# Kernel optimization log

Hardware: AMD Instinct MI355X
Metric: run time of the kernel (lower is better)

The kernel has to match this reference:

```python
import jax, jax.numpy as jnp
import numpy as np

EMBED_DIM = 1024
NUM_HEADS = 16
HEAD_DIM = EMBED_DIM // NUM_HEADS
SCALING = HEAD_DIM ** -0.5
NEG_FILL = -1e30


def setup_inputs() -> dict:
    key = jax.random.key(0)
    k1, k2, k3 = jax.random.split(key, 3)
    T, B, E = 2048, 4, EMBED_DIM
    query = jax.random.normal(k1, (T, B, E), dtype=jnp.float32)
    key_padding_mask = jnp.zeros((B, T), dtype=bool)  # 1 = padded key
    # xavier_uniform-like init
    lim_in = (6.0 / (3 * E + E)) ** 0.5
    in_proj_weight = jax.random.uniform(k2, (3 * E, E), minval=-lim_in, maxval=lim_in, dtype=jnp.float32)
    in_proj_bias = jnp.zeros((3 * E,), dtype=jnp.float32)
    lim_out = (6.0 / (E + E)) ** 0.5
    out_w = jax.random.uniform(k3, (E, E), minval=-lim_out, maxval=lim_out, dtype=jnp.float32)
    out_b = jnp.zeros((E,), dtype=jnp.float32)
    return {"query": query, "key_padding_mask": key_padding_mask,
            "in_proj_weight": in_proj_weight, "in_proj_bias": in_proj_bias,
            "out_w": out_w, "out_b": out_b}


def reference(query, key_padding_mask, in_proj_weight, in_proj_bias, out_w, out_b):
    T, B, E = query.shape
    H, D = NUM_HEADS, HEAD_DIM
    # fused in-projection (self-attention: qkv from same input)
    qkv = query @ in_proj_weight.T + in_proj_bias  # [T,B,3E]
    q, k, v = jnp.split(qkv, 3, axis=-1)
    q = q * SCALING
    q = q.reshape(T, B, H, D)
    k = k.reshape(T, B, H, D)
    v = v.reshape(T, B, H, D)
    # attention scores [B,H,T,S]
    scores = jnp.einsum('tbhd,sbhd->bhts', q, k)
    scores = jnp.where(key_padding_mask[:, None, None, :], NEG_FILL, scores)
    attn_w = jax.nn.softmax(scores, axis=-1)  # [B,H,T,S]
    # weighted sum of values -> [T,B,E]
    attn = jnp.einsum('bhts,sbhd->tbhd', attn_w, v).reshape(T, B, E)
    attn = attn @ out_w.T + out_b
    attn_w_avg = jnp.sum(attn_w, axis=1) / H  # [B,T,S]
    return attn, attn_w_avg
```

## Files before the change

### kernel.cpp

```cpp
#include <hip/hip_runtime.h>
#include <stdint.h>

#define QSCALE 0.18033688011112042f

typedef unsigned short u16;
typedef unsigned int u32;
typedef __attribute__((ext_vector_type(8))) __bf16 bf16x8;
typedef __attribute__((ext_vector_type(4))) float f32x4;
typedef __attribute__((ext_vector_type(16))) float f32x16;
typedef __attribute__((ext_vector_type(8))) u16 u16x8;
typedef __attribute__((ext_vector_type(4))) u32 u32x4;

__device__ __forceinline__ void gl_lds16(const void* g, void* l) {
  __builtin_amdgcn_global_load_lds(
      (const __attribute__((address_space(1))) void*)g,
      (__attribute__((address_space(3))) void*)l, 16, 0, 0);
}

__device__ __forceinline__ u16 f2bf(float f) {
  unsigned int u = __float_as_uint(f);
  u += 0x7FFFu + ((u >> 16) & 1u);
  return (u16)(u >> 16);
}

extern "C" __global__ __launch_bounds__(256) void cvt_f32_bf16(
    const float* __restrict__ src, u16* __restrict__ dst, int n) {
  int i = (blockIdx.x * 256 + threadIdx.x) * 4;
  if (i >= n) return;
  float4 v = *(const float4*)(src + i);
  ushort4 o;
  o.x = f2bf(v.x); o.y = f2bf(v.y); o.z = f2bf(v.z); o.w = f2bf(v.w);
  *(ushort4*)(dst + i) = o;
}

extern "C" __global__ __launch_bounds__(256) void gemm_qkv(
    const u16* __restrict__ X, const u16* __restrict__ W,
    const float* __restrict__ bias,
    u16* __restrict__ qb, u16* __restrict__ kb, u16* __restrict__ vtb) {
  const int tid = threadIdx.x;
  const int w = tid >> 6, lane = tid & 63;
  const int lg = lane >> 4, ll = lane & 15;
  const int wm = w >> 1, wn = w & 1;
  const int row0A = blockIdx.x * 128;
  const int row0B = blockIdx.y * 128;

  __shared__ __align__(16) u16 As[2][128 * 32];
  __shared__ __align__(16) u16 Bs[2][128 * 32];

  f32x4 acc[4][4] = {};

  const int r_st = tid >> 2;
  const int cb_st = (tid & 3) * 16;

#pragma unroll
  for (int it = 0; it < 2; ++it) {
    gl_lds16((const char*)X + ((size_t)(row0A + it * 64 + r_st) * 1024) * 2 + cb_st,
             (char*)&As[0][0] + it * 4096 + w * 1024);
    gl_lds16((const char*)W + ((size_t)(row0B + it * 64 + r_st) * 1024) * 2 + cb_st,
             (char*)&Bs[0][0] + it * 4096 + w * 1024);
  }

  for (int kt = 0; kt < 32; ++kt) {
    const int cur = kt & 1;
    asm volatile("s_waitcnt vmcnt(0)" ::: "memory");
    __syncthreads();
    if (kt + 1 < 32) {
      const int k0 = (kt + 1) * 32;
#pragma unroll
      for (int it = 0; it < 2; ++it) {
        gl_lds16((const char*)X + ((size_t)(row0A + it * 64 + r_st) * 1024 + k0) * 2 + cb_st,
                 (char*)&As[cur ^ 1][0] + it * 4096 + w * 1024);
        gl_lds16((const char*)W + ((size_t)(row0B + it * 64 + r_st) * 1024 + k0) * 2 + cb_st,
                 (char*)&Bs[cur ^ 1][0] + it * 4096 + w * 1024);
      }
    }
    const u16* Ab = &As[cur][0];
    const u16* Bb = &Bs[cur][0];
    const int kc = lg * 8;
    bf16x8 a[4], bfr[4];
#pragma unroll
    for (int i = 0; i < 4; ++i)
      a[i] = *(const bf16x8*)(Ab + (wm * 64 + i * 16 + ll) * 32 + kc);
#pragma unroll
    for (int j = 0; j < 4; ++j)
      bfr[j] = *(const bf16x8*)(Bb + (wn * 64 + j * 16 + ll) * 32 + kc);
#pragma unroll
    for (int i = 0; i < 4; ++i)
#pragma unroll
      for (int j = 0; j < 4; ++j)
        acc[i][j] = __builtin_amdgcn_mfma_f32_16x16x32_bf16(a[i], bfr[j], acc[i][j], 0, 0, 0);
  }

  const int which = row0B >> 10;
  if (which == 2) {
#pragma unroll
    for (int j = 0; j < 4; ++j) {
      const int n = row0B + wn * 64 + j * 16 + ll;
      const float bv = bias[n];
      const int n2 = n & 1023;
      const int hh = n2 >> 6, dd = n2 & 63;
#pragma unroll
      for (int i = 0; i < 4; ++i)
#pragma unroll
        for (int r = 0; r < 4; ++r) {
          const int m = row0A + wm * 64 + i * 16 + lg * 4 + r;
          const int tt = m >> 2, bb = m & 3;
          vtb[(((size_t)(bb * 16 + hh)) * 64 + dd) * 2048 + tt] =
              f2bf(acc[i][j][r] + bv);
        }
    }
  } else {
    u16* dst = which == 0 ? qb : kb;
    const float scl = which == 0 ? QSCALE : 1.0f;
#pragma unroll
    for (int j = 0; j < 4; ++j) {
      const int n = row0B + wn * 64 + j * 16 + ll;
      const float bv = bias[n];
      const int n2 = n & 1023;
      const int hh = n2 >> 6, dd = n2 & 63;
#pragma unroll
      for (int i = 0; i < 4; ++i)
#pragma unroll
        for (int r = 0; r < 4; ++r) {
          const int m = row0A + wm * 64 + i * 16 + lg * 4 + r;
          const int tt = m >> 2, bb = m & 3;
          dst[((size_t)(bb * 16 + hh) * 2048 + tt) * 64 + dd] =
              f2bf((acc[i][j][r] + bv) * scl);
        }
    }
  }
}

extern "C" __global__ __launch_bounds__(256, 3) void flash_fwd(
    const u16* __restrict__ q, const u16* __restrict__ k,
    const u16* __restrict__ vt, const unsigned char* __restrict__ mask,
    u16* __restrict__ attn_pre, float* __restrict__ stat_il) {
  const int lb = ((blockIdx.x & 7) << 7) + (blockIdx.x >> 3);
  const int bh = lb >> 4, tt = lb & 15;
  const int b = bh >> 4, hd = bh & 15;
  const int t0 = tt * 128;
  const int tid = threadIdx.x, w = tid >> 6, lane = tid & 63;
  const int hl = lane >> 5;
  const int l31 = lane & 31;

  __shared__ __align__(16) u16 Ks[3][64 * 64];
  __shared__ __align__(16) u16 Vs[3][64 * 64];
  __shared__ __align__(16) unsigned char Ms[2048];

  const int qrow = t0 + w * 32 + l31;
  const u16* qp = q + ((size_t)bh * 2048 + qrow) * 64 + hl * 8;
  bf16x8 qreg[4];
#pragma unroll
  for (int kg = 0; kg < 4; ++kg) qreg[kg] = *(const bf16x8*)(qp + kg * 16);

  f32x16 po[2] = {};
  float lsum = 0.f;

  const int slot_r = tid >> 3;
  const int slot_c8 = (tid & 7) ^ (slot_r & 7);

#define STAGE3(buf, s0_)                                                       \
  do {                                                                         \
    _Pragma("unroll") for (int it2 = 0; it2 < 2; ++it2) {                      \
      const int rr = it2 * 32 + slot_r;                                        \
      gl_lds16((const char*)k +                                                \
                   (((size_t)bh * 2048 + (s0_) + rr) * 64 + slot_c8 * 8) * 2,  \
               (char*)&Ks[buf][0] + it2 * 4096 + w * 1024);                    \
      gl_lds16((const char*)vt +                                               \
                   (((size_t)bh * 64 + rr) * 2048 + (s0_) + slot_c8 * 8) * 2,  \
               (char*)&Vs[buf][0] + it2 * 4096 + w * 1024);                    \
    }                                                                          \
  } while (0)

  if (w < 2)
    gl_lds16((const char*)mask + b * 2048 + w * 1024 + lane * 16,
             (char*)Ms + w * 1024);
  STAGE3(0, 0);
  STAGE3(1, 64);

  for (int t = 0; t < 32; ++t) {
    if (t < 31) {
      asm volatile("s_waitcnt vmcnt(4)" ::: "memory");
    } else {
      asm volatile("s_waitcnt vmcnt(0)" ::: "memory");
    }
    __builtin_amdgcn_s_barrier();
    if (t + 2 < 32) STAGE3((t + 2) % 3, (t + 2) * 64);

    const int s0 = t * 64;
    const int cur = t % 3;
    const char* Kb = (const char*)&Ks[cur][0];
    const char* Vb = (const char*)&Vs[cur][0];

    u32 mq[8];
#pragma unroll
    for (int kt = 0; kt < 2; ++kt)
#pragma unroll
      for (int j = 0; j < 4; ++j)
        mq[kt * 4 + j] =
            *(const u32*)(Ms + s0 + kt * 32 + j * 8 + hl * 4);
    const u32 anym = mq[0] | mq[1] | mq[2] | mq[3] | mq[4] | mq[5] | mq[6] | mq[7];

#pragma unroll
    for (int kt = 0; kt < 2; ++kt) {
      f32x16 z = {};
      const int key = kt * 32 + l31;
#pragma unroll
      for (int kg = 0; kg < 4; ++kg) {
        const bf16x8 kf = *(const bf16x8*)(
            Kb + key * 128 + ((((kg << 1) | hl) ^ (key & 7)) << 4));
        z = __builtin_amdgcn_mfma_f32_32x32x16_bf16(kf, qreg[kg], z, 0, 0, 0);
      }

      float ps[16];
#pragma unroll
      for (int r = 0; r < 16; ++r) ps[r] = __builtin_amdgcn_exp2f(z[r]);
      if (__any(anym != 0)) {
#pragma unroll
        for (int r = 0; r < 16; ++r)
          if ((mq[kt * 4 + (r >> 2)] >> ((r & 3) * 8)) & 0xFFu) ps[r] = 0.f;
      }
#pragma unroll
      for (int r = 0; r < 16; ++r) lsum += ps[r];

      u32 w8[8];
#pragma unroll
      for (int j = 0; j < 4; ++j) {
        asm("v_cvt_pk_bf16_f32 %0, %1, %2"
            : "=v"(w8[2 * j]) : "v"(ps[4 * j]), "v"(ps[4 * j + 1]));
        asm("v_cvt_pk_bf16_f32 %0, %1, %2"
            : "=v"(w8[2 * j + 1]) : "v"(ps[4 * j + 2]), "v"(ps[4 * j + 3]));
      }

#pragma unroll
      for (int f = 0; f < 2; ++f) {
        u32 d0 = w8[4 * f], d1 = w8[4 * f + 1];
        u32 s0w = w8[4 * f + 2], s1w = w8[4 * f + 3];
        asm volatile("v_permlane32_swap_b32 %0, %1" : "+v"(d0), "+v"(s0w));
        asm volatile("v_permlane32_swap_b32 %0, %1" : "+v"(d1), "+v"(s1w));
        const bf16x8 pa = __builtin_bit_cast(bf16x8, (u32x4){d0, d1, s0w, s1w});
        const int g = kt * 2 + f;
#pragma unroll
        for (int dt = 0; dt < 2; ++dt) {
          const int d = dt * 32 + l31;
          const bf16x8 vf = *(const bf16x8*)(
              Vb + d * 128 + ((((g << 1) | hl) ^ (d & 7)) << 4));
          po[dt] = __builtin_amdgcn_mfma_f32_32x32x16_bf16(pa, vf, po[dt], 0, 0, 0);
        }
      }
    }
  }

  lsum += __shfl_xor(lsum, 32, 64);
  const float linv = 1.0f / lsum;
  if (lane < 32)
    stat_il[(size_t)bh * 2048 + t0 + w * 32 + lane] = linv;

#pragma unroll
  for (int r = 0; r < 16; ++r) {
    const int qi = (r & 3) + 8 * (r >> 2) + 4 * hl;
    const float lv = __shfl(linv, qi, 64);
    const int trow = t0 + w * 32 + qi;
#pragma unroll
    for (int dt = 0; dt < 2; ++dt) {
      const int dd = dt * 32 + l31;
      attn_pre[((size_t)(trow * 4 + b)) * 1024 + hd * 64 + dd] =
          f2bf(po[dt][r] * lv);
    }
  }
#undef STAGE3
}

extern "C" __global__ __launch_bounds__(256, 3) void wavg(
    const u16* __restrict__ q, const u16* __restrict__ k,
    const unsigned char* __restrict__ mask,
    const float* __restrict__ stat_il, float* __restrict__ wout) {
  const int lb = ((blockIdx.x & 7) << 8) + (blockIdx.x >> 3);
  const int b = lb >> 9, tt = (lb >> 5) & 15, st = lb & 31;
  const int t0 = tt * 128, s0 = st * 64;
  const int tid = threadIdx.x, w = tid >> 6, lane = tid & 63;
  const int hl = lane >> 5;
  const int l31 = lane & 31;

  __shared__ __align__(16) u16 Qs[2][128 * 64];
  __shared__ __align__(16) u16 Ks2[2][64 * 64];

  const int slot_r8 = tid >> 3;
  const int slot_c8 = (tid & 7) ^ (slot_r8 & 7);

  u32 mq[8];
#pragma unroll
  for (int kt = 0; kt < 2; ++kt)
#pragma unroll
    for (int j = 0; j < 4; ++j)
      mq[kt * 4 + j] = *(const u32*)(mask + b * 2048 + s0 + kt * 32 + j * 8 + hl * 4);
  const u32 anym = mq[0] | mq[1] | mq[2] | mq[3] | mq[4] | mq[5] | mq[6] | mq[7];
  const bool domask = __any(anym != 0);

#define STAGE_W(buf, hh)                                                       \
  do {                                                                         \
    const size_t qo_ = (size_t)(b * 16 + (hh)) * 2048;                         \
    _Pragma("unroll") for (int i2 = 0; i2 < 4; ++i2) {                         \
      const int rr = i2 * 32 + slot_r8;                                        \
      gl_lds16((const char*)q + ((qo_ + t0 + rr) * 64 + slot_c8 * 8) * 2,      \
               (char*)&Qs[buf][0] + i2 * 4096 + w * 1024);                     \
    }                                                                          \
    _Pragma("unroll") for (int i2 = 0; i2 < 2; ++i2) {                         \
      const int rr = i2 * 32 + slot_r8;                                        \
      gl_lds16((const char*)k + ((qo_ + s0 + rr) * 64 + slot_c8 * 8) * 2,      \
               (char*)&Ks2[buf][0] + i2 * 4096 + w * 1024);                    \
    }                                                                          \
  } while (0)

  STAGE_W(0, 0);
  asm volatile("s_waitcnt vmcnt(0)" ::: "memory");
  __syncthreads();

  float accw[32] = {};
  for (int h = 0; h < 16; ++h) {
    const int cur = h & 1;
    const float ilh =
        stat_il[(size_t)(b * 16 + h) * 2048 + t0 + w * 32 + l31];

    if (h + 1 < 16) STAGE_W(cur ^ 1, h + 1);

    const char* Qb = (const char*)&Qs[cur][0];
    const char* Kb = (const char*)&Ks2[cur][0];

    const int qr = w * 32 + l31;
    bf16x8 qf[4];
#pragma unroll
    for (int kg = 0; kg < 4; ++kg)
      qf[kg] = *(const bf16x8*)(
          Qb + qr * 128 + ((((kg << 1) | hl) ^ (qr & 7)) << 4));

#pragma unroll
    for (int kt = 0; kt < 2; ++kt) {
      f32x16 z = {};
      const int key = kt * 32 + l31;
#pragma unroll
      for (int kg = 0; kg < 4; ++kg) {
        const bf16x8 kf = *(const bf16x8*)(
            Kb + key * 128 + ((((kg << 1) | hl) ^ (key & 7)) << 4));
        z = __builtin_amdgcn_mfma_f32_32x32x16_bf16(kf, qf[kg], z, 0, 0, 0);
      }
      float ps[16];
#pragma unroll
      for (int r = 0; r < 16; ++r) ps[r] = __builtin_amdgcn_exp2f(z[r]);
      if (domask) {
#pragma unroll
        for (int r = 0; r < 16; ++r)
          if ((mq[kt * 4 + (r >> 2)] >> ((r & 3) * 8)) & 0xFFu) ps[r] = 0.f;
      }
#pragma unroll
      for (int r = 0; r < 16; ++r)
        accw[kt * 16 + r] = fmaf(ps[r], ilh, accw[kt * 16 + r]);
    }

    asm volatile("s_waitcnt vmcnt(0)" ::: "memory");
    __syncthreads();
  }

  float* tb = ((float*)&Qs[0][0]) + w * 2048;
#pragma unroll
  for (int kt = 0; kt < 2; ++kt)
#pragma unroll
    for (int j = 0; j < 4; ++j) {
      f32x4 qd;
#pragma unroll
      for (int e = 0; e < 4; ++e) qd[e] = accw[kt * 16 + 4 * j + e] * 0.0625f;
      const int slot = kt * 8 + 2 * j + hl;
      *(f32x4*)(tb + l31 * 64 + ((slot ^ (l31 & 7)) << 2)) = qd;
    }
  __syncthreads();
#pragma unroll
  for (int j2 = 0; j2 < 8; ++j2) {
    const int row = j2 * 4 + (lane >> 4);
    const int slot = lane & 15;
    const f32x4 v = *(const f32x4*)(tb + row * 64 + ((slot ^ (row & 7)) << 2));
    *(f32x4*)(wout + ((size_t)b * 2048 + t0 + w * 32 + row) * 2048 + s0 +
              slot * 4) = v;
  }
#undef STAGE_W
}

extern "C" __global__ __launch_bounds__(256) void gemm_out(
    const u16* __restrict__ A, const u16* __restrict__ W,
    const float* __restrict__ bias, float* __restrict__ out) {
  const int tid = threadIdx.x;
  const int w = tid >> 6, lane = tid & 63;
  const int lg = lane >> 4, ll = lane & 15;
  const int wm = w >> 1, wn = w & 1;
  const int row0A = blockIdx.x * 128;
  const int row0B = blockIdx.y * 128;

  __shared__ __align__(16) u16 As[2][128 * 32];
  __shared__ __align__(16) u16 Bs[2][128 * 32];

  f32x4 acc[4][4] = {};
  const int r_st = tid >> 2;
  const int cb_st = (tid & 3) * 16;

#pragma unroll
  for (int it = 0; it < 2; ++it) {
    gl_lds16((const char*)A + ((size_t)(row0A + it * 64 + r_st) * 1024) * 2 + cb_st,
             (char*)&As[0][0] + it * 4096 + w * 1024);
    gl_lds16((const char*)W + ((size_t)(row0B + it * 64 + r_st) * 1024) * 2 + cb_st,
             (char*)&Bs[0][0] + it * 4096 + w * 1024);
  }

  for (int kt = 0; kt < 32; ++kt) {
    const int cur = kt & 1;
    asm volatile("s_waitcnt vmcnt(0)" ::: "memory");
    __syncthreads();
    if (kt + 1 < 32) {
      const int k0 = (kt + 1) * 32;
#pragma unroll
      for (int it = 0; it < 2; ++it) {
        gl_lds16((const char*)A + ((size_t)(row0A + it * 64 + r_st) * 1024 + k0) * 2 + cb_st,
                 (char*)&As[cur ^ 1][0] + it * 4096 + w * 1024);
        gl_lds16((const char*)W + ((size_t)(row0B + it * 64 + r_st) * 1024 + k0) * 2 + cb_st,
                 (char*)&Bs[cur ^ 1][0] + it * 4096 + w * 1024);
      }
    }
    const u16* Ab = &As[cur][0];
    const u16* Bb = &Bs[cur][0];
    const int kc = lg * 8;
    bf16x8 a[4], bfr[4];
#pragma unroll
    for (int i = 0; i < 4; ++i)
      a[i] = *(const bf16x8*)(Ab + (wm * 64 + i * 16 + ll) * 32 + kc);
#pragma unroll
    for (int j = 0; j < 4; ++j)
      bfr[j] = *(const bf16x8*)(Bb + (wn * 64 + j * 16 + ll) * 32 + kc);
#pragma unroll
    for (int i = 0; i < 4; ++i)
#pragma unroll
      for (int j = 0; j < 4; ++j)
        acc[i][j] = __builtin_amdgcn_mfma_f32_16x16x32_bf16(a[i], bfr[j], acc[i][j], 0, 0, 0);
  }

#pragma unroll
  for (int j = 0; j < 4; ++j) {
    const int n = row0B + wn * 64 + j * 16 + ll;
    const float bv = bias[n];
#pragma unroll
    for (int i = 0; i < 4; ++i)
#pragma unroll
      for (int r = 0; r < 4; ++r) {
        const int m = row0A + wm * 64 + i * 16 + lg * 4 + r;
        out[(size_t)m * 1024 + n] = acc[i][j][r] + bv;
      }
  }
}

extern "C" void kernel_launch(void* const* d_in, const int* in_sizes, int n_in,
                              void* d_out, int out_size, void* d_ws, size_t ws_size,
                              hipStream_t stream) {
  const float* query = (const float*)d_in[0];
  const unsigned char* mask = (const unsigned char*)d_in[1];
  const float* w_in = (const float*)d_in[2];
  const float* b_in = (const float*)d_in[3];
  const float* w_out = (const float*)d_in[4];
  const float* b_out = (const float*)d_in[5];

  float* out0 = (float*)d_out;
  float* outw = out0 + (size_t)8388608;

  char* ws = (char*)d_ws;
  u16* Xbf   = (u16*)(ws + 0);
  u16* Wqkv  = (u16*)(ws + 16777216);
  u16* Woutb = (u16*)(ws + 23068672);
  u16* qb    = (u16*)(ws + 25165824);
  u16* kb    = (u16*)(ws + 41943040);
  u16* vtb   = (u16*)(ws + 75497472);
  u16* ap    = (u16*)(ws + 92274688);
  float* sil = (float*)(ws + 109051904);

  cvt_f32_bf16<<<8192, 256, 0, stream>>>(query, Xbf, 8388608);
  cvt_f32_bf16<<<3072, 256, 0, stream>>>(w_in, Wqkv, 3145728);
  cvt_f32_bf16<<<1024, 256, 0, stream>>>(w_out, Woutb, 1048576);
  gemm_qkv<<<dim3(64, 24), 256, 0, stream>>>(Xbf, Wqkv, b_in, qb, kb, vtb);
  flash_fwd<<<1024, 256, 0, stream>>>(qb, kb, vtb, mask, ap, sil);
  wavg<<<2048, 256, 0, stream>>>(qb, kb, mask, sil, outw);
  gemm_out<<<dim3(64, 8), 256, 0, stream>>>(ap, Woutb, b_out, out0);
}
```

Before: 305.6 us.

## Merge fp32-to-bf16 conversions into one launch and transpose V separately

The three fp32-to-bf16 conversion launches are merged into a single kernel that picks its source by index range, writing into contiguous workspace regions. The QKV GEMM epilogue no longer does a strided, uncoalesced transposed store for V. It writes V in the same head-major layout as Q and K, and a new LDS-tiled transpose kernel produces the V^T layout the flash kernel expects. This trades the scattered 2-byte stores for an extra kernel launch plus an extra read and write of V.

Result: faster. 282.9 us (-7.4%).

```diff
diff --git a/kernel.cpp b/kernel.cpp
--- a/kernel.cpp
+++ b/kernel.cpp
@@ -23,11 +23,20 @@
   return (u16)(u >> 16);
 }
 
-extern "C" __global__ __launch_bounds__(256) void cvt_f32_bf16(
-    const float* __restrict__ src, u16* __restrict__ dst, int n) {
+extern "C" __global__ __launch_bounds__(256) void cvt_all(
+    const float* __restrict__ query, const float* __restrict__ w_in,
+    const float* __restrict__ w_out, u16* __restrict__ dst) {
   int i = (blockIdx.x * 256 + threadIdx.x) * 4;
-  if (i >= n) return;
-  float4 v = *(const float4*)(src + i);
+  const float* src;
+  int off;
+  if (i < 8388608) {
+    src = query; off = i;
+  } else if (i < 11534336) {
+    src = w_in; off = i - 8388608;
+  } else {
+    src = w_out; off = i - 11534336;
+  }
+  float4 v = *(const float4*)(src + off);
   ushort4 o;
   o.x = f2bf(v.x); o.y = f2bf(v.y); o.z = f2bf(v.z); o.w = f2bf(v.w);
   *(ushort4*)(dst + i) = o;
@@ -36,7 +45,7 @@
 extern "C" __global__ __launch_bounds__(256) void gemm_qkv(
     const u16* __restrict__ X, const u16* __restrict__ W,
     const float* __restrict__ bias,
-    u16* __restrict__ qb, u16* __restrict__ kb, u16* __restrict__ vtb) {
+    u16* __restrict__ qb, u16* __restrict__ kb, u16* __restrict__ vb) {
   const int tid = threadIdx.x;
   const int w = tid >> 6, lane = tid & 63;
   const int lg = lane >> 4, ll = lane & 15;
@@ -92,42 +101,49 @@
   }
 
   const int which = row0B >> 10;
-  if (which == 2) {
-#pragma unroll
-    for (int j = 0; j < 4; ++j) {
-      const int n = row0B + wn * 64 + j * 16 + ll;
-      const float bv = bias[n];
-      const int n2 = n & 1023;
-      const int hh = n2 >> 6, dd = n2 & 63;
-#pragma unroll
-      for (int i = 0; i < 4; ++i)
-#pragma unroll
-        for (int r = 0; r < 4; ++r) {
-          const int m = row0A + wm * 64 + i * 16 + lg * 4 + r;
-          const int tt = m >> 2, bb = m & 3;
-          vtb[(((size_t)(bb * 16 + hh)) * 64 + dd) * 2048 + tt] =
-              f2bf(acc[i][j][r] + bv);
-        }
-    }
-  } else {
-    u16* dst = which == 0 ? qb : kb;
-    const float scl = which == 0 ? QSCALE : 1.0f;
-#pragma unroll
-    for (int j = 0; j < 4; ++j) {
-      const int n = row0B + wn * 64 + j * 16 + ll;
-      const float bv = bias[n];
-      const int n2 = n & 1023;
-      const int hh = n2 >> 6, dd = n2 & 63;
-#pragma unroll
-      for (int i = 0; i < 4; ++i)
-#pragma unroll
-        for (int r = 0; r < 4; ++r) {
-          const int m = row0A + wm * 64 + i * 16 + lg * 4 + r;
-          const int tt = m >> 2, bb = m & 3;
-          dst[((size_t)(bb * 16 + hh) * 2048 + tt) * 64 + dd] =
-              f2bf((acc[i][j][r] + bv) * scl);
-        }
-    }
+  u16* dst = which == 0 ? qb : (which == 1 ? kb : vb);
+  const float scl = which == 0 ? QSCALE : 1.0f;
+#pragma unroll
+  for (int j = 0; j < 4; ++j) {
+    const int n = row0B + wn * 64 + j * 16 + ll;
+    const float bv = bias[n];
+    const int n2 = n & 1023;
+    const int hh = n2 >> 6, dd = n2 & 63;
+#pragma unroll
+    for (int i = 0; i < 4; ++i)
+#pragma unroll
+      for (int r = 0; r < 4; ++r) {
+        const int m = row0A + wm * 64 + i * 16 + lg * 4 + r;
+        const int tt = m >> 2, bb = m & 3;
+        dst[((size_t)(bb * 16 + hh) * 2048 + tt) * 64 + dd] = f2bf((acc[i][j][r] + bv) * scl);
+      }
+  }
+}
+
+extern "C" __global__ __launch_bounds__(256) void transpose_v(
+    const u16* __restrict__ v, u16* __restrict__ vt) {
+  const int blk = blockIdx.x;
+  const int bh = blk >> 5, tt = blk & 31;
+  const int t0 = tt * 64;
+  const int tid = threadIdx.x;
+  __shared__ __align__(16) u16 tile[64][72];
+  const u16* src = v + ((size_t)bh * 2048 + t0) * 64;
+#pragma unroll
+  for (int it = 0; it < 2; ++it) {
+    const int r = it * 32 + (tid >> 3);
+    const int c = (tid & 7) * 8;
+    *(u16x8*)(&tile[r][c]) = *(const u16x8*)(src + (size_t)r * 64 + c);
+  }
+  __syncthreads();
+  u16* dstb = vt + (size_t)bh * 64 * 2048 + t0;
+#pragma unroll
+  for (int it = 0; it < 2; ++it) {
+    const int d = it * 32 + (tid >> 3);
+    const int s = (tid & 7) * 8;
+    u16x8 o;
+#pragma unroll
+    for (int jj = 0; jj < 8; ++jj) o[jj] = tile[s + jj][d];
+    *(u16x8*)(dstb + (size_t)d * 2048 + s) = o;
   }
 }
 
@@ -473,14 +489,14 @@
   u16* Woutb = (u16*)(ws + 23068672);
   u16* qb    = (u16*)(ws + 25165824);
   u16* kb    = (u16*)(ws + 41943040);
+  u16* vb    = (u16*)(ws + 58720256);
   u16* vtb   = (u16*)(ws + 75497472);
   u16* ap    = (u16*)(ws + 92274688);
   float* sil = (float*)(ws + 109051904);
 
-  cvt_f32_bf16<<<8192, 256, 0, stream>>>(query, Xbf, 8388608);
-  cvt_f32_bf16<<<3072, 256, 0, stream>>>(w_in, Wqkv, 3145728);
-  cvt_f32_bf16<<<1024, 256, 0, stream>>>(w_out, Woutb, 1048576);
-  gemm_qkv<<<dim3(64, 24), 256, 0, stream>>>(Xbf, Wqkv, b_in, qb, kb, vtb);
+  cvt_all<<<12288, 256, 0, stream>>>(query, w_in, w_out, Xbf);
+  gemm_qkv<<<dim3(64, 24), 256, 0, stream>>>(Xbf, Wqkv, b_in, qb, kb, vb);
+  transpose_v<<<2048, 256, 0, stream>>>(vb, vtb);
   flash_fwd<<<1024, 256, 0, stream>>>(qb, kb, vtb, mask, ap, sil);
   wavg<<<2048, 256, 0, stream>>>(qb, kb, mask, sil, outw);
   gemm_out<<<dim3(64, 8), 256, 0, stream>>>(ap, Woutb, b_out, out0);
```
